# Optimization experiments

Measured on AMD Instinct MI355X. Metric: run time of the kernel, lower is better.

The kernel has to match this reference:

```python
import jax, jax.numpy as jnp
import numpy as np

HEADS = 8
DIM_HEAD = 64
QUERY_DIM = 512
INNER = HEADS * DIM_HEAD
T = 16
MAX_REL = 16  # == temporal_length
SCALE = DIM_HEAD ** -0.5


def _rel_idx(length_q, length_k):
    rq = jnp.arange(length_q)
    rk = jnp.arange(length_k)
    dist = rk[None, :] - rq[:, None]
    return jnp.clip(dist, -MAX_REL, MAX_REL) + MAX_REL  # [Tq, Tk] in [0, 2*MAX_REL]


def setup_inputs() -> dict:
    key = jax.random.key(0)
    ks = jax.random.split(key, 8)
    B = 2048
    s = 0.02
    return {
        "x": jax.random.normal(ks[0], (B, T, QUERY_DIM), dtype=jnp.float32),
        "Wq": jax.random.normal(ks[1], (QUERY_DIM, INNER), dtype=jnp.float32) * s,
        "Wk": jax.random.normal(ks[2], (QUERY_DIM, INNER), dtype=jnp.float32) * s,
        "Wv": jax.random.normal(ks[3], (QUERY_DIM, INNER), dtype=jnp.float32) * s,
        "Wo": jax.random.normal(ks[4], (INNER, QUERY_DIM), dtype=jnp.float32) * s,
        "bo": jnp.zeros((QUERY_DIM,), dtype=jnp.float32),
        "rel_k_table": jax.random.normal(ks[5], (2 * MAX_REL + 1, DIM_HEAD), dtype=jnp.float32) * s,
        "rel_v_table": jax.random.normal(ks[6], (2 * MAX_REL + 1, DIM_HEAD), dtype=jnp.float32) * s,
    }


def reference(x, Wq, Wk, Wv, Wo, bo, rel_k_table, rel_v_table):
    B, N, _ = x.shape
    # projections (Linear without bias)
    def split_heads(t):
        return t.reshape(B, N, HEADS, DIM_HEAD).transpose(0, 2, 1, 3)  # [B, H, N, D]
    q = split_heads(x @ Wq)
    k = split_heads(x @ Wk)
    v = split_heads(x @ Wv)

    sim = jnp.einsum('bhid,bhjd->bhij', q, k) * SCALE
    idx = _rel_idx(N, N)                     # [N, N]
    k2 = rel_k_table[idx]                    # [N, N, D]
    sim = sim + jnp.einsum('bhtd,tsd->bhts', q, k2) * SCALE

    attn = jax.nn.softmax(sim, axis=-1)
    out = jnp.einsum('bhij,bhjd->bhid', attn, v)
    v2 = rel_v_table[idx]                    # [N, N, D]
    out = out + jnp.einsum('bhts,tsd->bhtd', attn, v2)

    out = out.transpose(0, 2, 1, 3).reshape(B, N, INNER)
    return out @ Wo + bo
```

## Files before the change

### kernel.cpp

```cpp
#include <hip/hip_runtime.h>
#include <stdint.h>


using bf16x8 = __attribute__((ext_vector_type(8))) short;
using f32x4  = __attribute__((ext_vector_type(4))) float;

#define AS3P(p) ((__attribute__((address_space(3))) void*)(p))
#define AS1P(p) ((const __attribute__((address_space(1))) void*)(p))

__device__ __forceinline__ uint16_t f2bf(float f) {
  unsigned int x = __builtin_bit_cast(unsigned int, f);
  x += 0x7fffu + ((x >> 16) & 1u);
  return (uint16_t)(x >> 16);
}

__global__ void cast_kernel(const float* __restrict__ in, uint16_t* __restrict__ out, int n8) {
  int i = blockIdx.x * 256 + threadIdx.x;
  if (i >= n8) return;
  float4 a = ((const float4*)in)[i * 2];
  float4 b = ((const float4*)in)[i * 2 + 1];
  uint4 r;
  r.x = (uint32_t)f2bf(a.x) | ((uint32_t)f2bf(a.y) << 16);
  r.y = (uint32_t)f2bf(a.z) | ((uint32_t)f2bf(a.w) << 16);
  r.z = (uint32_t)f2bf(b.x) | ((uint32_t)f2bf(b.y) << 16);
  r.w = (uint32_t)f2bf(b.z) | ((uint32_t)f2bf(b.w) << 16);
  ((uint4*)out)[i] = r;
}

__global__ void transpose_cast(const float* __restrict__ src, uint16_t* __restrict__ dst) {
  __shared__ float tile[32][33];
  int tx = threadIdx.x, ty = threadIdx.y;
  int c0 = blockIdx.x * 32, r0 = blockIdx.y * 32;
  #pragma unroll
  for (int k = 0; k < 4; ++k)
    tile[ty + 8 * k][tx] = src[(r0 + ty + 8 * k) * 512 + c0 + tx];
  __syncthreads();
  #pragma unroll
  for (int k = 0; k < 4; ++k)
    dst[(c0 + ty + 8 * k) * 512 + r0 + tx] = f2bf(tile[tx][ty + 8 * k]);
}

template<int OUT_BF16, int KDIM>
__global__ __launch_bounds__(512, 2) void gemm256(
    const uint16_t* __restrict__ A, const uint16_t* __restrict__ B,
    void* __restrict__ C, const float* __restrict__ bias, int N, int nbx) {
  constexpr int NT = KDIM / 32;
  static_assert(NT >= 4, "need >=4 K-tiles");
  __shared__ __align__(16) uint16_t lds[4][2][8192];
  const int tid = threadIdx.x;
  const int w = tid >> 6, l = tid & 63;
  const int lr = l & 15, kc = l >> 4;
  const int wm = w >> 2, wn = w & 3;
  const int cpx = gridDim.x >> 3;
  const int id = blockIdx.x;
  const int swz = (id & 7) * cpx + (id >> 3);
  const int by = swz / nbx, bx = swz - by * nbx;
  const int mBase = by * 256, nBase = bx * 256;
  const int g8 = l >> 3;
  const int sub = (l & 7) ^ g8;
  const int srow = w * 32 + g8 * 2 + (sub >> 2);
  const int scol = (sub & 3) * 8;
  const uint16_t* gA0 = A + (size_t)(mBase + srow) * KDIM + scol;
  const uint16_t* gA1 = gA0 + 16 * KDIM;
  const uint16_t* gB0 = B + (size_t)(nBase + srow) * KDIM + scol;
  const uint16_t* gB1 = gB0 + 16 * KDIM;
  int offA[8], offB[4];
  #pragma unroll
  for (int m = 0; m < 8; ++m) {
    int row = wm * 128 + m * 16 + lr;
    int rp = row >> 1, sb = ((row & 1) << 2) | kc;
    offA[m] = rp * 128 + (sb ^ (rp & 7)) * 16;
  }
  #pragma unroll
  for (int n = 0; n < 4; ++n) {
    int row = wn * 64 + n * 16 + lr;
    int rp = row >> 1, sb = ((row & 1) << 2) | kc;
    offB[n] = rp * 128 + (sb ^ (rp & 7)) * 16;
  }
  f32x4 acc[8][4] = {};
  #pragma unroll
  for (int pt = 0; pt < 3; ++pt) {
    uint16_t* dA = &lds[pt][0][w * 1024];
    uint16_t* dB = &lds[pt][1][w * 1024];
    __builtin_amdgcn_global_load_lds(AS1P(gA0 + pt * 32), AS3P(dA),       16, 0, 0);
    __builtin_amdgcn_global_load_lds(AS1P(gA1 + pt * 32), AS3P(dA + 512), 16, 0, 0);
    __builtin_amdgcn_global_load_lds(AS1P(gB0 + pt * 32), AS3P(dB),       16, 0, 0);
    __builtin_amdgcn_global_load_lds(AS1P(gB1 + pt * 32), AS3P(dB + 512), 16, 0, 0);
  }
  asm volatile("s_waitcnt vmcnt(8)" ::: "memory");
  __builtin_amdgcn_s_barrier();

  #pragma unroll 4
  for (int t = 0; t < NT; ++t) {
    const int bi = t & 3;
    const int si = (t + 3) & 3;
    const char* bufA = (const char*)&lds[bi][0][0];
    const char* bufB = (const char*)&lds[bi][1][0];
    if (t + 3 < NT) {
      uint16_t* dA = &lds[si][0][w * 1024];
      __builtin_amdgcn_global_load_lds(AS1P(gA0 + (t + 3) * 32), AS3P(dA),       16, 0, 0);
      __builtin_amdgcn_global_load_lds(AS1P(gA1 + (t + 3) * 32), AS3P(dA + 512), 16, 0, 0);
    }
    if (t + 3 < NT)       asm volatile("s_waitcnt vmcnt(6)" ::: "memory");
    else if (t + 3 == NT) asm volatile("s_waitcnt vmcnt(4)" ::: "memory");
    else if (t + 2 == NT) asm volatile("s_waitcnt vmcnt(0)" ::: "memory");
    bf16x8 a0 = *(const bf16x8*)(bufA + offA[0]);
    bf16x8 a1 = *(const bf16x8*)(bufA + offA[1]);
    bf16x8 a2 = *(const bf16x8*)(bufA + offA[2]);
    bf16x8 a3 = *(const bf16x8*)(bufA + offA[3]);
    bf16x8 b0 = *(const bf16x8*)(bufB + offB[0]);
    bf16x8 b1 = *(const bf16x8*)(bufB + offB[1]);
    bf16x8 b2 = *(const bf16x8*)(bufB + offB[2]);
    bf16x8 b3 = *(const bf16x8*)(bufB + offB[3]);
    __builtin_amdgcn_sched_barrier(0);
    __builtin_amdgcn_s_barrier();
    asm volatile("s_waitcnt lgkmcnt(0)" ::: "memory");
    __builtin_amdgcn_sched_barrier(0);
    __builtin_amdgcn_s_setprio(1);
    acc[0][0] = __builtin_amdgcn_mfma_f32_16x16x32_bf16(a0, b0, acc[0][0], 0, 0, 0);
    acc[0][1] = __builtin_amdgcn_mfma_f32_16x16x32_bf16(a0, b1, acc[0][1], 0, 0, 0);
    acc[0][2] = __builtin_amdgcn_mfma_f32_16x16x32_bf16(a0, b2, acc[0][2], 0, 0, 0);
    acc[0][3] = __builtin_amdgcn_mfma_f32_16x16x32_bf16(a0, b3, acc[0][3], 0, 0, 0);
    acc[1][0] = __builtin_amdgcn_mfma_f32_16x16x32_bf16(a1, b0, acc[1][0], 0, 0, 0);
    acc[1][1] = __builtin_amdgcn_mfma_f32_16x16x32_bf16(a1, b1, acc[1][1], 0, 0, 0);
    acc[1][2] = __builtin_amdgcn_mfma_f32_16x16x32_bf16(a1, b2, acc[1][2], 0, 0, 0);
    acc[1][3] = __builtin_amdgcn_mfma_f32_16x16x32_bf16(a1, b3, acc[1][3], 0, 0, 0);
    acc[2][0] = __builtin_amdgcn_mfma_f32_16x16x32_bf16(a2, b0, acc[2][0], 0, 0, 0);
    acc[2][1] = __builtin_amdgcn_mfma_f32_16x16x32_bf16(a2, b1, acc[2][1], 0, 0, 0);
    acc[2][2] = __builtin_amdgcn_mfma_f32_16x16x32_bf16(a2, b2, acc[2][2], 0, 0, 0);
    acc[2][3] = __builtin_amdgcn_mfma_f32_16x16x32_bf16(a2, b3, acc[2][3], 0, 0, 0);
    acc[3][0] = __builtin_amdgcn_mfma_f32_16x16x32_bf16(a3, b0, acc[3][0], 0, 0, 0);
    acc[3][1] = __builtin_amdgcn_mfma_f32_16x16x32_bf16(a3, b1, acc[3][1], 0, 0, 0);
    acc[3][2] = __builtin_amdgcn_mfma_f32_16x16x32_bf16(a3, b2, acc[3][2], 0, 0, 0);
    acc[3][3] = __builtin_amdgcn_mfma_f32_16x16x32_bf16(a3, b3, acc[3][3], 0, 0, 0);
    __builtin_amdgcn_s_setprio(0);
    __builtin_amdgcn_sched_barrier(0);
    __builtin_amdgcn_s_barrier();
    if (t + 3 < NT) {
      uint16_t* dB = &lds[si][1][w * 1024];
      __builtin_amdgcn_global_load_lds(AS1P(gB0 + (t + 3) * 32), AS3P(dB),       16, 0, 0);
      __builtin_amdgcn_global_load_lds(AS1P(gB1 + (t + 3) * 32), AS3P(dB + 512), 16, 0, 0);
    }
    bf16x8 a4 = *(const bf16x8*)(bufA + offA[4]);
    bf16x8 a5 = *(const bf16x8*)(bufA + offA[5]);
    bf16x8 a6 = *(const bf16x8*)(bufA + offA[6]);
    bf16x8 a7 = *(const bf16x8*)(bufA + offA[7]);
    __builtin_amdgcn_sched_barrier(0);
    __builtin_amdgcn_s_barrier();
    asm volatile("s_waitcnt lgkmcnt(0)" ::: "memory");
    __builtin_amdgcn_sched_barrier(0);
    __builtin_amdgcn_s_setprio(1);
    acc[4][0] = __builtin_amdgcn_mfma_f32_16x16x32_bf16(a4, b0, acc[4][0], 0, 0, 0);
    acc[4][1] = __builtin_amdgcn_mfma_f32_16x16x32_bf16(a4, b1, acc[4][1], 0, 0, 0);
    acc[4][2] = __builtin_amdgcn_mfma_f32_16x16x32_bf16(a4, b2, acc[4][2], 0, 0, 0);
    acc[4][3] = __builtin_amdgcn_mfma_f32_16x16x32_bf16(a4, b3, acc[4][3], 0, 0, 0);
    acc[5][0] = __builtin_amdgcn_mfma_f32_16x16x32_bf16(a5, b0, acc[5][0], 0, 0, 0);
    acc[5][1] = __builtin_amdgcn_mfma_f32_16x16x32_bf16(a5, b1, acc[5][1], 0, 0, 0);
    acc[5][2] = __builtin_amdgcn_mfma_f32_16x16x32_bf16(a5, b2, acc[5][2], 0, 0, 0);
    acc[5][3] = __builtin_amdgcn_mfma_f32_16x16x32_bf16(a5, b3, acc[5][3], 0, 0, 0);
    acc[6][0] = __builtin_amdgcn_mfma_f32_16x16x32_bf16(a6, b0, acc[6][0], 0, 0, 0);
    acc[6][1] = __builtin_amdgcn_mfma_f32_16x16x32_bf16(a6, b1, acc[6][1], 0, 0, 0);
    acc[6][2] = __builtin_amdgcn_mfma_f32_16x16x32_bf16(a6, b2, acc[6][2], 0, 0, 0);
    acc[6][3] = __builtin_amdgcn_mfma_f32_16x16x32_bf16(a6, b3, acc[6][3], 0, 0, 0);
    acc[7][0] = __builtin_amdgcn_mfma_f32_16x16x32_bf16(a7, b0, acc[7][0], 0, 0, 0);
    acc[7][1] = __builtin_amdgcn_mfma_f32_16x16x32_bf16(a7, b1, acc[7][1], 0, 0, 0);
    acc[7][2] = __builtin_amdgcn_mfma_f32_16x16x32_bf16(a7, b2, acc[7][2], 0, 0, 0);
    acc[7][3] = __builtin_amdgcn_mfma_f32_16x16x32_bf16(a7, b3, acc[7][3], 0, 0, 0);
    __builtin_amdgcn_s_setprio(0);
    __builtin_amdgcn_sched_barrier(0);
    __builtin_amdgcn_s_barrier();
  }
  #pragma unroll
  for (int m = 0; m < 8; ++m)
    #pragma unroll
    for (int n = 0; n < 4; ++n) {
      const int col = nBase + wn * 64 + n * 16 + lr;
      #pragma unroll
      for (int r = 0; r < 4; ++r) {
        const int row = mBase + wm * 128 + m * 16 + kc * 4 + r;
        if (OUT_BF16) ((uint16_t*)C)[(size_t)row * N + col] = f2bf(acc[m][n][r]);
        else          ((float*)C)[(size_t)row * N + col]    = acc[m][n][r] + bias[col];
      }
    }
}

__global__ __launch_bounds__(256) void attn_kernel(
    const uint16_t* __restrict__ qkv,
    const float* __restrict__ relk, const float* __restrict__ relv,
    uint16_t* __restrict__ outA) {
  __shared__ __align__(16) uint16_t relkS[33 * 72];
  __shared__ __align__(16) uint16_t relvT[64 * 40];
  __shared__ __align__(16) uint16_t vT[4][64 * 24];
  __shared__ float attnS[4][16 * 17];
  const int tid = threadIdx.x;
  for (int e = tid; e < 33 * 64; e += 256) {
    int j = e >> 6, d = e & 63;
    relkS[j * 72 + d] = f2bf(relk[e]);
    relvT[d * 40 + j] = f2bf(relv[e]);
  }
  const int w = tid >> 6, l = tid & 63;
  const int bh = blockIdx.x * 4 + w;
  const int b = bh >> 3, h = bh & 7;
  const int rowBase = b * 16;
  const int lr = l & 15, kc = l >> 4;
  const uint16_t* qrow = qkv + (size_t)(rowBase + lr) * 1536 + h * 64;
  bf16x8 aq0 = *(const bf16x8*)(qrow + kc * 8);
  bf16x8 aq1 = *(const bf16x8*)(qrow + 32 + kc * 8);
  const uint16_t* krow = qrow + 512;
  bf16x8 bk0 = *(const bf16x8*)(krow + kc * 8);
  bf16x8 bk1 = *(const bf16x8*)(krow + 32 + kc * 8);
  {
    const int s = l >> 2, dg = l & 3;
    const uint16_t* vrow = qkv + (size_t)(rowBase + s) * 1536 + 1024 + h * 64 + dg * 16;
    uint4 v0 = *(const uint4*)vrow;
    uint4 v1 = *(const uint4*)(vrow + 8);
    uint16_t tmp[16];
    *(uint4*)(tmp) = v0; *(uint4*)(tmp + 8) = v1;
    #pragma unroll
    for (int i = 0; i < 16; ++i)
      vT[w][(dg * 16 + i) * 24 + s] = tmp[i];
  }
  __syncthreads();
  const f32x4 zero = {0.f, 0.f, 0.f, 0.f};
  f32x4 sim = __builtin_amdgcn_mfma_f32_16x16x32_bf16(aq0, bk0, zero, 0, 0, 0);
  sim = __builtin_amdgcn_mfma_f32_16x16x32_bf16(aq1, bk1, sim, 0, 0, 0);
  bf16x8 rka0 = *(const bf16x8*)(relkS + lr * 72 + kc * 8);
  bf16x8 rka1 = *(const bf16x8*)(relkS + lr * 72 + 32 + kc * 8);
  bf16x8 rkb0 = *(const bf16x8*)(relkS + (16 + lr) * 72 + kc * 8);
  bf16x8 rkb1 = *(const bf16x8*)(relkS + (16 + lr) * 72 + 32 + kc * 8);
  f32x4 rqa = __builtin_amdgcn_mfma_f32_16x16x32_bf16(aq0, rka0, zero, 0, 0, 0);
  rqa = __builtin_amdgcn_mfma_f32_16x16x32_bf16(aq1, rka1, rqa, 0, 0, 0);
  f32x4 rqb = __builtin_amdgcn_mfma_f32_16x16x32_bf16(aq0, rkb0, zero, 0, 0, 0);
  rqb = __builtin_amdgcn_mfma_f32_16x16x32_bf16(aq1, rkb1, rqb, 0, 0, 0);
  #pragma unroll
  for (int r = 0; r < 4; ++r) {
    const int t = kc * 4 + r;
    const int j = lr - t + 16;
    const int src = (l & 48) | (j & 15);
    const float va = __shfl(rqa[r], src, 64);
    const float vb = __shfl(rqb[r], src, 64);
    const float rqv = (j < 16) ? va : vb;
    float sv = (sim[r] + rqv) * 0.125f;
    float m = sv;
    m = fmaxf(m, __shfl_xor(m, 1, 64));
    m = fmaxf(m, __shfl_xor(m, 2, 64));
    m = fmaxf(m, __shfl_xor(m, 4, 64));
    m = fmaxf(m, __shfl_xor(m, 8, 64));
    const float p = __expf(sv - m);
    float su = p;
    su += __shfl_xor(su, 1, 64);
    su += __shfl_xor(su, 2, 64);
    su += __shfl_xor(su, 4, 64);
    su += __shfl_xor(su, 8, 64);
    attnS[w][t * 17 + lr] = p / su;
  }
  __syncthreads();
  const float* aS = attnS[w];
  bf16x8 attnA, w2A;
  #pragma unroll
  for (int i = 0; i < 8; ++i) {
    const int s1 = kc * 8 + i;
    attnA[i] = (s1 < 16) ? (short)f2bf(aS[lr * 17 + s1]) : (short)0;
    const int s2 = s1 + lr - 16;
    w2A[i] = (s2 >= 0 && s2 < 16) ? (short)f2bf(aS[lr * 17 + s2]) : (short)0;
  }
  #pragma unroll
  for (int dt = 0; dt < 4; ++dt) {
    bf16x8 vf  = *(const bf16x8*)(&vT[w][(dt * 16 + lr) * 24 + (kc & 1) * 8]);
    bf16x8 rvf = *(const bf16x8*)(&relvT[(dt * 16 + lr) * 40 + kc * 8]);
    f32x4 o = __builtin_amdgcn_mfma_f32_16x16x32_bf16(w2A, rvf, zero, 0, 0, 0);
    o = __builtin_amdgcn_mfma_f32_16x16x32_bf16(attnA, vf, o, 0, 0, 0);
    #pragma unroll
    for (int r = 0; r < 4; ++r) {
      const int t = kc * 4 + r;
      outA[(size_t)(rowBase + t) * 512 + h * 64 + dt * 16 + lr] = f2bf(o[r]);
    }
  }
}

extern "C" void kernel_launch(void* const* d_in, const int* in_sizes, int n_in,
                              void* d_out, int out_size, void* d_ws, size_t ws_size,
                              hipStream_t stream) {
  const float* x    = (const float*)d_in[0];
  const float* Wq   = (const float*)d_in[1];
  const float* Wk   = (const float*)d_in[2];
  const float* Wv   = (const float*)d_in[3];
  const float* Wo   = (const float*)d_in[4];
  const float* bo   = (const float*)d_in[5];
  const float* relk = (const float*)d_in[6];
  const float* relv = (const float*)d_in[7];

  char* ws = (char*)d_ws;
  uint16_t* qkv   = (uint16_t*)ws;
  uint16_t* xbf   = (uint16_t*)(ws + 100663296);
  uint16_t* WqkvT = (uint16_t*)(ws + 134217728);
  uint16_t* WoT   = (uint16_t*)(ws + 135790592);
  uint16_t* attnO = xbf;

  cast_kernel<<<8192, 256, 0, stream>>>(x, xbf, 2097152);
  dim3 tb(32, 8);
  transpose_cast<<<dim3(16, 16), tb, 0, stream>>>(Wq, WqkvT);
  transpose_cast<<<dim3(16, 16), tb, 0, stream>>>(Wk, WqkvT + 262144);
  transpose_cast<<<dim3(16, 16), tb, 0, stream>>>(Wv, WqkvT + 524288);
  transpose_cast<<<dim3(16, 16), tb, 0, stream>>>(Wo, WoT);
  gemm256<1, 512><<<dim3(768), dim3(512), 0, stream>>>(xbf, WqkvT, (void*)qkv, nullptr, 1536, 6);
  attn_kernel<<<4096, 256, 0, stream>>>(qkv, relk, relv, attnO);
  gemm256<0, 512><<<dim3(256), dim3(512), 0, stream>>>(attnO, WoT, d_out, bo, 512, 2);
}
```

Before: 150.2 us.

## Fuse fp32-to-bf16 cast of x into QKV GEMM A-tile loads

Removes the standalone cast kernel for x and adds a GEMM variant that stages fp32 A tiles into LDS and converts them to bf16 in registers with packed convert instructions before MFMA. This drops one kernel launch and the bf16 intermediate write and read. In exchange, A tiles are twice as large in LDS and global reads, and reloaded across N-tiles, with a 3-stage buffer instead of 4. The attention kernel also moves to 512-thread blocks handling 8 heads each.

```diff
diff --git a/kernel.cpp b/kernel.cpp
--- a/kernel.cpp
+++ b/kernel.cpp
@@ -13,18 +13,16 @@
   x += 0x7fffu + ((x >> 16) & 1u);
   return (uint16_t)(x >> 16);
 }
-
-__global__ void cast_kernel(const float* __restrict__ in, uint16_t* __restrict__ out, int n8) {
-  int i = blockIdx.x * 256 + threadIdx.x;
-  if (i >= n8) return;
-  float4 a = ((const float4*)in)[i * 2];
-  float4 b = ((const float4*)in)[i * 2 + 1];
-  uint4 r;
-  r.x = (uint32_t)f2bf(a.x) | ((uint32_t)f2bf(a.y) << 16);
-  r.y = (uint32_t)f2bf(a.z) | ((uint32_t)f2bf(a.w) << 16);
-  r.z = (uint32_t)f2bf(b.x) | ((uint32_t)f2bf(b.y) << 16);
-  r.w = (uint32_t)f2bf(b.z) | ((uint32_t)f2bf(b.w) << 16);
-  ((uint4*)out)[i] = r;
+__device__ __forceinline__ uint32_t cvtpk(float lo, float hi) {
+  uint32_t r;
+  asm("v_cvt_pk_bf16_f32 %0, %1, %2" : "=v"(r) : "v"(lo), "v"(hi));
+  return r;
+}
+__device__ __forceinline__ bf16x8 packA(f32x4 lo, f32x4 hi) {
+  int4 r;
+  r.x = (int)cvtpk(lo[0], lo[1]); r.y = (int)cvtpk(lo[2], lo[3]);
+  r.z = (int)cvtpk(hi[0], hi[1]); r.w = (int)cvtpk(hi[2], hi[3]);
+  return __builtin_bit_cast(bf16x8, r);
 }
 
 __global__ void transpose_cast(const float* __restrict__ src, uint16_t* __restrict__ dst) {
@@ -38,6 +36,163 @@
   #pragma unroll
   for (int k = 0; k < 4; ++k)
     dst[(c0 + ty + 8 * k) * 512 + r0 + tx] = f2bf(tile[tx][ty + 8 * k]);
+}
+
+template<int KDIM>
+__global__ __launch_bounds__(512, 2) void gemm_f32a(
+    const float* __restrict__ A, const uint16_t* __restrict__ B,
+    uint16_t* __restrict__ C, int N, int nbx) {
+  constexpr int NT = KDIM / 32;
+  __shared__ __align__(16) float    ldsA[3][8192];
+  __shared__ __align__(16) uint16_t ldsB[3][8192];
+  const int tid = threadIdx.x;
+  const int w = tid >> 6, l = tid & 63;
+  const int lr = l & 15, kc = l >> 4;
+  const int wm = w >> 2, wn = w & 3;
+  const int cpx = gridDim.x >> 3;
+  const int id = blockIdx.x;
+  const int swz = (id & 7) * cpx + (id >> 3);
+  const int by = swz / nbx, bx = swz - by * nbx;
+  const int mBase = by * 256, nBase = bx * 256;
+  const int g8a = l >> 3;
+  const float* gA = A + (size_t)(mBase + w * 32 + g8a) * KDIM + ((l & 7) ^ g8a) * 4;
+  const int sub = (l & 7) ^ g8a;
+  const uint16_t* gB0 = B + (size_t)(nBase + w * 32 + g8a * 2 + (sub >> 2)) * KDIM + (sub & 3) * 8;
+  const uint16_t* gB1 = gB0 + 16 * KDIM;
+  int offA[8], offB[4];
+  #pragma unroll
+  for (int m = 0; m < 8; ++m) {
+    int row = wm * 128 + m * 16 + lr;
+    offA[m] = row * 128 + (((kc << 1) ^ (row & 7)) << 4);
+  }
+  #pragma unroll
+  for (int n = 0; n < 4; ++n) {
+    int row = wn * 64 + n * 16 + lr;
+    int rp = row >> 1, sb = ((row & 1) << 2) | kc;
+    offB[n] = rp * 128 + ((sb ^ (rp & 7)) << 4);
+  }
+  f32x4 acc[8][4] = {};
+
+#define STAGE_A1(t, bf) do { \
+    float* d = &ldsA[bf][w * 1024]; \
+    const float* s = gA + (t) * 32; \
+    __builtin_amdgcn_global_load_lds(AS1P(s),             AS3P(d),       16, 0, 0); \
+    __builtin_amdgcn_global_load_lds(AS1P(s + 8 * KDIM),  AS3P(d + 256), 16, 0, 0); \
+    __builtin_amdgcn_global_load_lds(AS1P(s + 16 * KDIM), AS3P(d + 512), 16, 0, 0); \
+    __builtin_amdgcn_global_load_lds(AS1P(s + 24 * KDIM), AS3P(d + 768), 16, 0, 0); \
+  } while (0)
+#define STAGE_B1(t, bf) do { \
+    uint16_t* d = &ldsB[bf][w * 1024]; \
+    __builtin_amdgcn_global_load_lds(AS1P(gB0 + (t) * 32), AS3P(d),       16, 0, 0); \
+    __builtin_amdgcn_global_load_lds(AS1P(gB1 + (t) * 32), AS3P(d + 512), 16, 0, 0); \
+  } while (0)
+
+  STAGE_A1(0, 0); STAGE_B1(0, 0);
+  STAGE_A1(1, 1); STAGE_B1(1, 1);
+  asm volatile("s_waitcnt vmcnt(6)" ::: "memory");
+  __builtin_amdgcn_s_barrier();
+
+  #pragma unroll
+  for (int t = 0; t < NT; ++t) {
+    const int bi = t % 3;
+    const int si = (t + 2) % 3;
+    const char* bufA = (const char*)&ldsA[bi][0];
+    const char* bufB = (const char*)&ldsB[bi][0];
+    if (t + 2 < NT) STAGE_A1(t + 2, si);
+    if (t < NT - 2)       asm volatile("s_waitcnt vmcnt(10)" ::: "memory");
+    else if (t == NT - 2) asm volatile("s_waitcnt vmcnt(6)" ::: "memory");
+    else                  asm volatile("s_waitcnt vmcnt(0)" ::: "memory");
+    f32x4 xa[8];
+    #pragma unroll
+    for (int m = 0; m < 4; ++m) {
+      xa[2 * m]     = *(const f32x4*)(bufA + offA[m]);
+      xa[2 * m + 1] = *(const f32x4*)(bufA + (offA[m] ^ 16));
+    }
+    bf16x8 b0 = *(const bf16x8*)(bufB + offB[0]);
+    bf16x8 b1 = *(const bf16x8*)(bufB + offB[1]);
+    bf16x8 b2 = *(const bf16x8*)(bufB + offB[2]);
+    bf16x8 b3 = *(const bf16x8*)(bufB + offB[3]);
+    __builtin_amdgcn_sched_barrier(0);
+    __builtin_amdgcn_s_barrier();
+    asm volatile("s_waitcnt lgkmcnt(0)" ::: "memory");
+    __builtin_amdgcn_sched_barrier(0);
+    __builtin_amdgcn_s_setprio(1);
+    {
+      bf16x8 a0 = packA(xa[0], xa[1]);
+      bf16x8 a1 = packA(xa[2], xa[3]);
+      bf16x8 a2 = packA(xa[4], xa[5]);
+      bf16x8 a3 = packA(xa[6], xa[7]);
+      acc[0][0] = __builtin_amdgcn_mfma_f32_16x16x32_bf16(a0, b0, acc[0][0], 0, 0, 0);
+      acc[0][1] = __builtin_amdgcn_mfma_f32_16x16x32_bf16(a0, b1, acc[0][1], 0, 0, 0);
+      acc[0][2] = __builtin_amdgcn_mfma_f32_16x16x32_bf16(a0, b2, acc[0][2], 0, 0, 0);
+      acc[0][3] = __builtin_amdgcn_mfma_f32_16x16x32_bf16(a0, b3, acc[0][3], 0, 0, 0);
+      acc[1][0] = __builtin_amdgcn_mfma_f32_16x16x32_bf16(a1, b0, acc[1][0], 0, 0, 0);
+      acc[1][1] = __builtin_amdgcn_mfma_f32_16x16x32_bf16(a1, b1, acc[1][1], 0, 0, 0);
+      acc[1][2] = __builtin_amdgcn_mfma_f32_16x16x32_bf16(a1, b2, acc[1][2], 0, 0, 0);
+      acc[1][3] = __builtin_amdgcn_mfma_f32_16x16x32_bf16(a1, b3, acc[1][3], 0, 0, 0);
+      acc[2][0] = __builtin_amdgcn_mfma_f32_16x16x32_bf16(a2, b0, acc[2][0], 0, 0, 0);
+      acc[2][1] = __builtin_amdgcn_mfma_f32_16x16x32_bf16(a2, b1, acc[2][1], 0, 0, 0);
+      acc[2][2] = __builtin_amdgcn_mfma_f32_16x16x32_bf16(a2, b2, acc[2][2], 0, 0, 0);
+      acc[2][3] = __builtin_amdgcn_mfma_f32_16x16x32_bf16(a2, b3, acc[2][3], 0, 0, 0);
+      acc[3][0] = __builtin_amdgcn_mfma_f32_16x16x32_bf16(a3, b0, acc[3][0], 0, 0, 0);
+      acc[3][1] = __builtin_amdgcn_mfma_f32_16x16x32_bf16(a3, b1, acc[3][1], 0, 0, 0);
+      acc[3][2] = __builtin_amdgcn_mfma_f32_16x16x32_bf16(a3, b2, acc[3][2], 0, 0, 0);
+      acc[3][3] = __builtin_amdgcn_mfma_f32_16x16x32_bf16(a3, b3, acc[3][3], 0, 0, 0);
+    }
+    __builtin_amdgcn_s_setprio(0);
+    __builtin_amdgcn_sched_barrier(0);
+    __builtin_amdgcn_s_barrier();
+    if (t + 2 < NT) STAGE_B1(t + 2, si);
+    f32x4 xb[8];
+    #pragma unroll
+    for (int m = 0; m < 4; ++m) {
+      xb[2 * m]     = *(const f32x4*)(bufA + offA[4 + m]);
+      xb[2 * m + 1] = *(const f32x4*)(bufA + (offA[4 + m] ^ 16));
+    }
+    __builtin_amdgcn_sched_barrier(0);
+    __builtin_amdgcn_s_barrier();
+    asm volatile("s_waitcnt lgkmcnt(0)" ::: "memory");
+    __builtin_amdgcn_sched_barrier(0);
+    __builtin_amdgcn_s_setprio(1);
+    {
+      bf16x8 a4 = packA(xb[0], xb[1]);
+      bf16x8 a5 = packA(xb[2], xb[3]);
+      bf16x8 a6 = packA(xb[4], xb[5]);
+      bf16x8 a7 = packA(xb[6], xb[7]);
+      acc[4][0] = __builtin_amdgcn_mfma_f32_16x16x32_bf16(a4, b0, acc[4][0], 0, 0, 0);
+      acc[4][1] = __builtin_amdgcn_mfma_f32_16x16x32_bf16(a4, b1, acc[4][1], 0, 0, 0);
+      acc[4][2] = __builtin_amdgcn_mfma_f32_16x16x32_bf16(a4, b2, acc[4][2], 0, 0, 0);
+      acc[4][3] = __builtin_amdgcn_mfma_f32_16x16x32_bf16(a4, b3, acc[4][3], 0, 0, 0);
+      acc[5][0] = __builtin_amdgcn_mfma_f32_16x16x32_bf16(a5, b0, acc[5][0], 0, 0, 0);
+      acc[5][1] = __builtin_amdgcn_mfma_f32_16x16x32_bf16(a5, b1, acc[5][1], 0, 0, 0);
+      acc[5][2] = __builtin_amdgcn_mfma_f32_16x16x32_bf16(a5, b2, acc[5][2], 0, 0, 0);
+      acc[5][3] = __builtin_amdgcn_mfma_f32_16x16x32_bf16(a5, b3, acc[5][3], 0, 0, 0);
+      acc[6][0] = __builtin_amdgcn_mfma_f32_16x16x32_bf16(a6, b0, acc[6][0], 0, 0, 0);
+      acc[6][1] = __builtin_amdgcn_mfma_f32_16x16x32_bf16(a6, b1, acc[6][1], 0, 0, 0);
+      acc[6][2] = __builtin_amdgcn_mfma_f32_16x16x32_bf16(a6, b2, acc[6][2], 0, 0, 0);
+      acc[6][3] = __builtin_amdgcn_mfma_f32_16x16x32_bf16(a6, b3, acc[6][3], 0, 0, 0);
+      acc[7][0] = __builtin_amdgcn_mfma_f32_16x16x32_bf16(a7, b0, acc[7][0], 0, 0, 0);
+      acc[7][1] = __builtin_amdgcn_mfma_f32_16x16x32_bf16(a7, b1, acc[7][1], 0, 0, 0);
+      acc[7][2] = __builtin_amdgcn_mfma_f32_16x16x32_bf16(a7, b2, acc[7][2], 0, 0, 0);
+      acc[7][3] = __builtin_amdgcn_mfma_f32_16x16x32_bf16(a7, b3, acc[7][3], 0, 0, 0);
+    }
+    __builtin_amdgcn_s_setprio(0);
+    __builtin_amdgcn_sched_barrier(0);
+    __builtin_amdgcn_s_barrier();
+  }
+#undef STAGE_A1
+#undef STAGE_B1
+  #pragma unroll
+  for (int m = 0; m < 8; ++m)
+    #pragma unroll
+    for (int n = 0; n < 4; ++n) {
+      const int col = nBase + wn * 64 + n * 16 + lr;
+      #pragma unroll
+      for (int r = 0; r < 4; ++r) {
+        const int row = mBase + wm * 128 + m * 16 + kc * 4 + r;
+        C[(size_t)row * N + col] = f2bf(acc[m][n][r]);
+      }
+    }
 }
 
 template<int OUT_BF16, int KDIM>
@@ -45,7 +200,6 @@
     const uint16_t* __restrict__ A, const uint16_t* __restrict__ B,
     void* __restrict__ C, const float* __restrict__ bias, int N, int nbx) {
   constexpr int NT = KDIM / 32;
-  static_assert(NT >= 4, "need >=4 K-tiles");
   __shared__ __align__(16) uint16_t lds[4][2][8192];
   const int tid = threadIdx.x;
   const int w = tid >> 6, l = tid & 63;
@@ -69,13 +223,13 @@
   for (int m = 0; m < 8; ++m) {
     int row = wm * 128 + m * 16 + lr;
     int rp = row >> 1, sb = ((row & 1) << 2) | kc;
-    offA[m] = rp * 128 + (sb ^ (rp & 7)) * 16;
+    offA[m] = rp * 128 + ((sb ^ (rp & 7)) << 4);
   }
   #pragma unroll
   for (int n = 0; n < 4; ++n) {
     int row = wn * 64 + n * 16 + lr;
     int rp = row >> 1, sb = ((row & 1) << 2) | kc;
-    offB[n] = rp * 128 + (sb ^ (rp & 7)) * 16;
+    offB[n] = rp * 128 + ((sb ^ (rp & 7)) << 4);
   }
   f32x4 acc[8][4] = {};
   #pragma unroll
@@ -89,7 +243,6 @@
   }
   asm volatile("s_waitcnt vmcnt(8)" ::: "memory");
   __builtin_amdgcn_s_barrier();
-
   #pragma unroll 4
   for (int t = 0; t < NT; ++t) {
     const int bi = t & 3;
@@ -184,22 +337,22 @@
     }
 }
 
-__global__ __launch_bounds__(256) void attn_kernel(
+__global__ __launch_bounds__(512) void attn_kernel(
     const uint16_t* __restrict__ qkv,
     const float* __restrict__ relk, const float* __restrict__ relv,
     uint16_t* __restrict__ outA) {
   __shared__ __align__(16) uint16_t relkS[33 * 72];
   __shared__ __align__(16) uint16_t relvT[64 * 40];
-  __shared__ __align__(16) uint16_t vT[4][64 * 24];
-  __shared__ float attnS[4][16 * 17];
+  __shared__ __align__(16) uint16_t vT[8][64 * 24];
+  __shared__ float attnS[8][16 * 17];
   const int tid = threadIdx.x;
-  for (int e = tid; e < 33 * 64; e += 256) {
+  for (int e = tid; e < 33 * 64; e += 512) {
     int j = e >> 6, d = e & 63;
     relkS[j * 72 + d] = f2bf(relk[e]);
     relvT[d * 40 + j] = f2bf(relv[e]);
   }
   const int w = tid >> 6, l = tid & 63;
-  const int bh = blockIdx.x * 4 + w;
+  const int bh = blockIdx.x * 8 + w;
   const int b = bh >> 3, h = bh & 7;
   const int rowBase = b * 16;
   const int lr = l & 15, kc = l >> 4;
@@ -292,18 +445,16 @@
 
   char* ws = (char*)d_ws;
   uint16_t* qkv   = (uint16_t*)ws;
-  uint16_t* xbf   = (uint16_t*)(ws + 100663296);
+  uint16_t* attnO = (uint16_t*)(ws + 100663296);
   uint16_t* WqkvT = (uint16_t*)(ws + 134217728);
   uint16_t* WoT   = (uint16_t*)(ws + 135790592);
-  uint16_t* attnO = xbf;
-
-  cast_kernel<<<8192, 256, 0, stream>>>(x, xbf, 2097152);
+
   dim3 tb(32, 8);
   transpose_cast<<<dim3(16, 16), tb, 0, stream>>>(Wq, WqkvT);
   transpose_cast<<<dim3(16, 16), tb, 0, stream>>>(Wk, WqkvT + 262144);
   transpose_cast<<<dim3(16, 16), tb, 0, stream>>>(Wv, WqkvT + 524288);
   transpose_cast<<<dim3(16, 16), tb, 0, stream>>>(Wo, WoT);
-  gemm256<1, 512><<<dim3(768), dim3(512), 0, stream>>>(xbf, WqkvT, (void*)qkv, nullptr, 1536, 6);
-  attn_kernel<<<4096, 256, 0, stream>>>(qkv, relk, relv, attnO);
+  gemm_f32a<512><<<dim3(768), dim3(512), 0, stream>>>(x, WqkvT, qkv, 1536, 6);
+  attn_kernel<<<2048, 512, 0, stream>>>(qkv, relk, relv, attnO);
   gemm256<0, 512><<<dim3(256), dim3(512), 0, stream>>>(attnO, WoT, d_out, bo, 512, 2);
 }
```

After: 162.5 us. +8.2%, slower.

## Stage bf16 outputs through LDS for vectorized stores; merge weight transposes

Applied to the files above, without the earlier changes.

The QKV GEMM epilogue and the attention kernel now write their bf16 results into a swizzled LDS tile, then emit 16-byte vector global stores instead of scattered 2-byte stores. The four weight transpose launches are merged into one launch indexed by blockIdx.z. The attention kernel doubles its block size to 8 waves, which halves how often each block reloads the relative-position tables. This adds LDS use (an extra 16KB in the GEMM, which may reduce occupancy) and some waitcnt barriers in the epilogue.

```diff
diff --git a/kernel.cpp b/kernel.cpp
--- a/kernel.cpp
+++ b/kernel.cpp
@@ -27,8 +27,13 @@
   ((uint4*)out)[i] = r;
 }
 
-__global__ void transpose_cast(const float* __restrict__ src, uint16_t* __restrict__ dst) {
+__global__ void transpose_cast4(const float* __restrict__ Wq, const float* __restrict__ Wk,
+                                const float* __restrict__ Wv, const float* __restrict__ Wo,
+                                uint16_t* __restrict__ WqkvT, uint16_t* __restrict__ WoT) {
   __shared__ float tile[32][33];
+  const int z = blockIdx.z;
+  const float* src = (z == 0) ? Wq : (z == 1) ? Wk : (z == 2) ? Wv : Wo;
+  uint16_t* dst = (z == 3) ? WoT : (WqkvT + z * 262144);
   int tx = threadIdx.x, ty = threadIdx.y;
   int c0 = blockIdx.x * 32, r0 = blockIdx.y * 32;
   #pragma unroll
@@ -45,8 +50,8 @@
     const uint16_t* __restrict__ A, const uint16_t* __restrict__ B,
     void* __restrict__ C, const float* __restrict__ bias, int N, int nbx) {
   constexpr int NT = KDIM / 32;
-  static_assert(NT >= 4, "need >=4 K-tiles");
   __shared__ __align__(16) uint16_t lds[4][2][8192];
+  __shared__ __align__(16) uint16_t ldsO[8][1024];
   const int tid = threadIdx.x;
   const int w = tid >> 6, l = tid & 63;
   const int lr = l & 15, kc = l >> 4;
@@ -69,13 +74,13 @@
   for (int m = 0; m < 8; ++m) {
     int row = wm * 128 + m * 16 + lr;
     int rp = row >> 1, sb = ((row & 1) << 2) | kc;
-    offA[m] = rp * 128 + (sb ^ (rp & 7)) * 16;
+    offA[m] = rp * 128 + ((sb ^ (rp & 7)) << 4);
   }
   #pragma unroll
   for (int n = 0; n < 4; ++n) {
     int row = wn * 64 + n * 16 + lr;
     int rp = row >> 1, sb = ((row & 1) << 2) | kc;
-    offB[n] = rp * 128 + (sb ^ (rp & 7)) * 16;
+    offB[n] = rp * 128 + ((sb ^ (rp & 7)) << 4);
   }
   f32x4 acc[8][4] = {};
   #pragma unroll
@@ -89,7 +94,6 @@
   }
   asm volatile("s_waitcnt vmcnt(8)" ::: "memory");
   __builtin_amdgcn_s_barrier();
-
   #pragma unroll 4
   for (int t = 0; t < NT; ++t) {
     const int bi = t & 3;
@@ -170,36 +174,61 @@
     __builtin_amdgcn_sched_barrier(0);
     __builtin_amdgcn_s_barrier();
   }
-  #pragma unroll
-  for (int m = 0; m < 8; ++m)
+  if (OUT_BF16) {
+    uint16_t* oW = &ldsO[w][0];
+    const int t2 = l >> 3, c2 = l & 7;
+    uint16_t* gO = (uint16_t*)C + (size_t)(mBase + wm * 128 + t2) * N + (nBase + wn * 64 + c2 * 8);
     #pragma unroll
-    for (int n = 0; n < 4; ++n) {
-      const int col = nBase + wn * 64 + n * 16 + lr;
+    for (int m = 0; m < 8; ++m) {
       #pragma unroll
-      for (int r = 0; r < 4; ++r) {
-        const int row = mBase + wm * 128 + m * 16 + kc * 4 + r;
-        if (OUT_BF16) ((uint16_t*)C)[(size_t)row * N + col] = f2bf(acc[m][n][r]);
-        else          ((float*)C)[(size_t)row * N + col]    = acc[m][n][r] + bias[col];
+      for (int n = 0; n < 4; ++n)
+        #pragma unroll
+        for (int r = 0; r < 4; ++r) {
+          const int tt = kc * 4 + r;
+          const int d = n * 16 + lr;
+          const int col = (((d >> 3) ^ (tt & 7)) << 3) | (d & 7);
+          oW[tt * 64 + col] = f2bf(acc[m][n][r]);
+        }
+      asm volatile("s_waitcnt lgkmcnt(0)" ::: "memory");
+      __builtin_amdgcn_sched_barrier(0);
+      bf16x8 s0 = *(const bf16x8*)(oW + t2 * 64 + (((c2 ^ (t2 & 7)) << 3)));
+      bf16x8 s1 = *(const bf16x8*)(oW + (8 + t2) * 64 + (((c2 ^ (t2 & 7)) << 3)));
+      *(bf16x8*)(gO + (size_t)(m * 16) * N) = s0;
+      *(bf16x8*)(gO + (size_t)(m * 16 + 8) * N) = s1;
+      asm volatile("s_waitcnt lgkmcnt(0)" ::: "memory");
+      __builtin_amdgcn_sched_barrier(0);
+    }
+  } else {
+    #pragma unroll
+    for (int m = 0; m < 8; ++m)
+      #pragma unroll
+      for (int n = 0; n < 4; ++n) {
+        const int col = nBase + wn * 64 + n * 16 + lr;
+        #pragma unroll
+        for (int r = 0; r < 4; ++r) {
+          const int row = mBase + wm * 128 + m * 16 + kc * 4 + r;
+          ((float*)C)[(size_t)row * N + col] = acc[m][n][r] + bias[col];
+        }
       }
-    }
-}
-
-__global__ __launch_bounds__(256) void attn_kernel(
+  }
+}
+
+__global__ __launch_bounds__(512) void attn_kernel(
     const uint16_t* __restrict__ qkv,
     const float* __restrict__ relk, const float* __restrict__ relv,
     uint16_t* __restrict__ outA) {
   __shared__ __align__(16) uint16_t relkS[33 * 72];
   __shared__ __align__(16) uint16_t relvT[64 * 40];
-  __shared__ __align__(16) uint16_t vT[4][64 * 24];
-  __shared__ float attnS[4][16 * 17];
+  __shared__ __align__(16) uint16_t vT[8][64 * 24];
+  __shared__ float attnS[8][16 * 17];
   const int tid = threadIdx.x;
-  for (int e = tid; e < 33 * 64; e += 256) {
+  for (int e = tid; e < 33 * 64; e += 512) {
     int j = e >> 6, d = e & 63;
     relkS[j * 72 + d] = f2bf(relk[e]);
     relvT[d * 40 + j] = f2bf(relv[e]);
   }
   const int w = tid >> 6, l = tid & 63;
-  const int bh = blockIdx.x * 4 + w;
+  const int bh = blockIdx.x * 8 + w;
   const int b = bh >> 3, h = bh & 7;
   const int rowBase = b * 16;
   const int lr = l & 15, kc = l >> 4;
@@ -264,18 +293,32 @@
     const int s2 = s1 + lr - 16;
     w2A[i] = (s2 >= 0 && s2 < 16) ? (short)f2bf(aS[lr * 17 + s2]) : (short)0;
   }
+  f32x4 o[4];
   #pragma unroll
   for (int dt = 0; dt < 4; ++dt) {
     bf16x8 vf  = *(const bf16x8*)(&vT[w][(dt * 16 + lr) * 24 + (kc & 1) * 8]);
     bf16x8 rvf = *(const bf16x8*)(&relvT[(dt * 16 + lr) * 40 + kc * 8]);
-    f32x4 o = __builtin_amdgcn_mfma_f32_16x16x32_bf16(w2A, rvf, zero, 0, 0, 0);
-    o = __builtin_amdgcn_mfma_f32_16x16x32_bf16(attnA, vf, o, 0, 0, 0);
+    o[dt] = __builtin_amdgcn_mfma_f32_16x16x32_bf16(w2A, rvf, zero, 0, 0, 0);
+    o[dt] = __builtin_amdgcn_mfma_f32_16x16x32_bf16(attnA, vf, o[dt], 0, 0, 0);
+  }
+  asm volatile("s_waitcnt lgkmcnt(0)" ::: "memory");
+  __builtin_amdgcn_sched_barrier(0);
+  uint16_t* oW = &vT[w][0];
+  #pragma unroll
+  for (int dt = 0; dt < 4; ++dt)
     #pragma unroll
     for (int r = 0; r < 4; ++r) {
       const int t = kc * 4 + r;
-      outA[(size_t)(rowBase + t) * 512 + h * 64 + dt * 16 + lr] = f2bf(o[r]);
+      const int chunk = dt * 2 + (lr >> 3);
+      oW[t * 64 + ((chunk ^ (t & 7)) << 3) + (lr & 7)] = f2bf(o[dt][r]);
     }
-  }
+  asm volatile("s_waitcnt lgkmcnt(0)" ::: "memory");
+  __builtin_amdgcn_sched_barrier(0);
+  const int t2 = l >> 3, c2 = l & 7;
+  bf16x8 s0 = *(const bf16x8*)(oW + t2 * 64 + ((c2 ^ (t2 & 7)) << 3));
+  bf16x8 s1 = *(const bf16x8*)(oW + (8 + t2) * 64 + ((c2 ^ (t2 & 7)) << 3));
+  *(bf16x8*)(outA + (size_t)(rowBase + t2) * 512 + h * 64 + c2 * 8) = s0;
+  *(bf16x8*)(outA + (size_t)(rowBase + 8 + t2) * 512 + h * 64 + c2 * 8) = s1;
 }
 
 extern "C" void kernel_launch(void* const* d_in, const int* in_sizes, int n_in,
@@ -298,12 +341,8 @@
   uint16_t* attnO = xbf;
 
   cast_kernel<<<8192, 256, 0, stream>>>(x, xbf, 2097152);
-  dim3 tb(32, 8);
-  transpose_cast<<<dim3(16, 16), tb, 0, stream>>>(Wq, WqkvT);
-  transpose_cast<<<dim3(16, 16), tb, 0, stream>>>(Wk, WqkvT + 262144);
-  transpose_cast<<<dim3(16, 16), tb, 0, stream>>>(Wv, WqkvT + 524288);
-  transpose_cast<<<dim3(16, 16), tb, 0, stream>>>(Wo, WoT);
+  transpose_cast4<<<dim3(16, 16, 4), dim3(32, 8), 0, stream>>>(Wq, Wk, Wv, Wo, WqkvT, WoT);
   gemm256<1, 512><<<dim3(768), dim3(512), 0, stream>>>(xbf, WqkvT, (void*)qkv, nullptr, 1536, 6);
-  attn_kernel<<<4096, 256, 0, stream>>>(qkv, relk, relv, attnO);
+  attn_kernel<<<2048, 512, 0, stream>>>(qkv, relk, relv, attnO);
   gemm256<0, 512><<<dim3(256), dim3(512), 0, stream>>>(attnO, WoT, d_out, bo, 512, 2);
 }
```

New measurement: 141.9 us. 1.06x faster.
